# Optimization experiments

Hardware: AMD Instinct MI355X
Metric: run time of the kernel (lower is better)

Reference implementation:

```python
import jax, jax.numpy as jnp
import numpy as np

B, S, DIN, DOUT = 2, 4096, 4096, 11008

def setup_inputs() -> dict:
    key = jax.random.key(0)
    k1, k2, k3 = jax.random.split(key, 3)
    x = jax.random.normal(k1, (B, S, DIN), dtype=jnp.float32)
    # kaiming-uniform-ish full-precision weight
    bound_w = 1.0 / np.sqrt(DIN)
    weight = jax.random.uniform(k2, (DOUT, DIN), dtype=jnp.float32, minval=-bound_w, maxval=bound_w)
    bias = jax.random.uniform(k3, (DOUT,), dtype=jnp.float32, minval=-bound_w, maxval=bound_w)
    return {"x": x, "weight": weight, "bias": bias}

def reference(x, weight, bias):
    # Binarize weight to {-1, 0, +1} via sign (matches torch.sign), scale by mean |w| (detached)
    binary_w = jnp.sign(weight)                                  # [DOUT, DIN]
    scale = jax.lax.stop_gradient(jnp.mean(jnp.abs(weight)))    # scalar
    w_q = binary_w * scale
    # F.linear: x @ w_q.T + bias
    out = jnp.einsum('bsi,oi->bso', x, w_q) + bias               # [B, S, DOUT]
    return out
```

## Files before the change

### kernel.cpp

```cpp
#include <hip/hip_runtime.h>

#define MDIM 8192
#define KDIM 4096
#define NDIM 11008

#define NBLK_W 1024

typedef float f32x4 __attribute__((ext_vector_type(4)));
typedef int   i32x4 __attribute__((ext_vector_type(4)));
typedef char  c4    __attribute__((ext_vector_type(4)));

#define GAS __attribute__((address_space(1)))
#define LAS __attribute__((address_space(3)))

__global__ __launch_bounds__(256) void k_convert_w(const float* __restrict__ w,
                                                   char* __restrict__ wq,
                                                   float* __restrict__ partials) {
  const int n4 = (NDIM * KDIM) / 4;
  const int stride = gridDim.x * blockDim.x;
  float s = 0.f;
  for (int i = blockIdx.x * blockDim.x + threadIdx.x; i < n4; i += stride) {
    f32x4 v = ((const f32x4*)w)[i];
    s += fabsf(v.x) + fabsf(v.y) + fabsf(v.z) + fabsf(v.w);
    c4 q;
    q.x = v.x > 0.f ? 1 : (v.x < 0.f ? -1 : 0);
    q.y = v.y > 0.f ? 1 : (v.y < 0.f ? -1 : 0);
    q.z = v.z > 0.f ? 1 : (v.z < 0.f ? -1 : 0);
    q.w = v.w > 0.f ? 1 : (v.w < 0.f ? -1 : 0);
    ((c4*)wq)[i] = q;
  }
  #pragma unroll
  for (int off = 32; off > 0; off >>= 1) s += __shfl_down(s, off, 64);
  __shared__ float red[4];
  if ((threadIdx.x & 63) == 0) red[threadIdx.x >> 6] = s;
  __syncthreads();
  if (threadIdx.x == 0) partials[blockIdx.x] = red[0] + red[1] + red[2] + red[3];
}

__global__ __launch_bounds__(256) void k_scale(const float* __restrict__ partials,
                                               float* __restrict__ scale) {
  float s = 0.f;
  for (int i = threadIdx.x; i < NBLK_W; i += 256) s += partials[i];
  #pragma unroll
  for (int off = 32; off > 0; off >>= 1) s += __shfl_down(s, off, 64);
  __shared__ float red[4];
  if ((threadIdx.x & 63) == 0) red[threadIdx.x >> 6] = s;
  __syncthreads();
  if (threadIdx.x == 0)
    *scale = (red[0] + red[1] + red[2] + red[3]) / (float)((size_t)NDIM * KDIM);
}

__global__ __launch_bounds__(256) void k_convert_x(const float* __restrict__ x,
                                                   char* __restrict__ xq,
                                                   float* __restrict__ sx) {
  const int row = blockIdx.x;
  const float* xr = x + (size_t)row * KDIM;
  const int t = (int)threadIdx.x;
  f32x4 v[4];
  float mx = 0.f;
  #pragma unroll
  for (int j = 0; j < 4; ++j) {
    v[j] = *(const f32x4*)(xr + j * 1024 + t * 4);
    mx = fmaxf(mx, fmaxf(fmaxf(fabsf(v[j].x), fabsf(v[j].y)),
                         fmaxf(fabsf(v[j].z), fabsf(v[j].w))));
  }
  #pragma unroll
  for (int off = 32; off > 0; off >>= 1) mx = fmaxf(mx, __shfl_xor(mx, off, 64));
  __shared__ float red[4];
  __shared__ float bmax;
  if ((t & 63) == 0) red[t >> 6] = mx;
  __syncthreads();
  if (t == 0) {
    float m2 = fmaxf(fmaxf(red[0], red[1]), fmaxf(red[2], red[3]));
    m2 = fmaxf(m2, 1e-20f);
    bmax = m2;
    sx[row] = m2 * (1.f / 127.f);
  }
  __syncthreads();
  const float r = 127.f / bmax;
  #pragma unroll
  for (int j = 0; j < 4; ++j) {
    int a = __float2int_rn(v[j].x * r), b = __float2int_rn(v[j].y * r);
    int c = __float2int_rn(v[j].z * r), d = __float2int_rn(v[j].w * r);
    a = a > 127 ? 127 : (a < -127 ? -127 : a);
    b = b > 127 ? 127 : (b < -127 ? -127 : b);
    c = c > 127 ? 127 : (c < -127 ? -127 : c);
    d = d > 127 ? 127 : (d < -127 ? -127 : d);
    c4 q; q.x = (char)a; q.y = (char)b; q.z = (char)c; q.w = (char)d;
    *(c4*)(xq + (size_t)row * KDIM + j * 1024 + t * 4) = q;
  }
}


#define BAR()  __builtin_amdgcn_s_barrier()
#define SB0()  __builtin_amdgcn_sched_barrier(0)
#define PRIO1() __builtin_amdgcn_s_setprio(1)
#define PRIO0() __builtin_amdgcn_s_setprio(0)
#define VM(N)  asm volatile("s_waitcnt vmcnt(" #N ")" ::: "memory")

#define STAGE(GP, ROWB, LDSOFF, HALF, KT) do {                                        \
  const char* _s = (GP) + (size_t)((ROWB) + (HALF)*128 + srow) * KDIM                 \
                   + (KT)*64 + scol;                                                  \
  char* _d = lds + (LDSOFF) + (HALF)*8192 + tid*16;                                   \
  __builtin_amdgcn_global_load_lds((const GAS unsigned int*)_s,                       \
                                   (LAS unsigned int*)_d, 16, 0, 0);                  \
} while (0)

#define LOAD_B2(DST, BUF, NB)                                                         \
  _Pragma("unroll") for (int ni = 0; ni < 2; ++ni)                                    \
    DST[ni] = *(const i32x4*)&lds[(BUF)*32768 + 16384 + bWOff + ((NB)+ni)*1024        \
                                  + rowoff + rcol];

#define LOAD_A(DST, BUF, MQ)                                                          \
  _Pragma("unroll") for (int mi = 0; mi < 4; ++mi)                                    \
    DST[mi] = *(const i32x4*)&lds[(BUF)*32768 + aWOff + (MQ)*4096 + mi*1024           \
                                  + rowoff + rcol];

#define MFMA8(AF, MB, BQ, NB)                                                         \
  _Pragma("unroll") for (int mi = 0; mi < 4; ++mi)                                    \
  _Pragma("unroll") for (int ni = 0; ni < 2; ++ni)                                    \
    acc[(MB)+mi][(NB)+ni] = __builtin_amdgcn_mfma_i32_16x16x64_i8(                    \
        AF[mi], BQ[ni], acc[(MB)+mi][(NB)+ni], 0, 0, 0);

__global__ __launch_bounds__(512, 2) void k_gemm256(const char* __restrict__ A,
                                                    const char* __restrict__ B,
                                                    const float* __restrict__ bias,
                                                    const float* __restrict__ sx,
                                                    const float* __restrict__ scale_p,
                                                    float* __restrict__ C) {
  extern __shared__ char lds[];

  const int nTn = NDIM / 256;
  const int nwg = (MDIM / 256) * nTn;
  int wg = (int)blockIdx.x;
  wg = (wg & 7) * (nwg / 8) + (wg >> 3);
  const int tm = wg / nTn;
  const int tn = wg % nTn;

  const int tid  = (int)threadIdx.x;
  const int lane = tid & 63;
  const int wave = tid >> 6;
  const int wm   = wave >> 2;
  const int wn   = wave & 3;
  const int l15  = lane & 15;

  const int rowoff = l15 * 64;
  const int rcol = ((lane >> 4) << 4) ^ (((l15 >> 1) & 3) << 4);
  const int srow = tid >> 2;
  const int scol = ((tid & 3) << 4) ^ (((tid >> 3) & 3) << 4);

  const int aWOff = wm * 8192;
  const int bWOff = (wn >> 1) * 8192 + (wn & 1) * 4096;
  const int aRow = tm * 256;
  const int bRow = tn * 256;

  i32x4 acc[8][4];
  #pragma unroll
  for (int i = 0; i < 8; ++i)
    #pragma unroll
    for (int j = 0; j < 4; ++j) acc[i][j] = i32x4{0, 0, 0, 0};

  i32x4 af[4], bq01[2], bq23[2];

  STAGE(B, bRow, 16384, 0, 0);
  STAGE(B, bRow, 16384, 1, 0);
  STAGE(A, aRow, 0,     0, 0);
  STAGE(A, aRow, 0,     1, 0);
  STAGE(B, bRow, 49152, 0, 1);
  STAGE(B, bRow, 49152, 1, 1);
  VM(2);
  SB0();
  BAR();
  LOAD_A(af, 0, 0); LOAD_B2(bq01, 0, 0);

  #pragma unroll 1
  for (int i = 0; i < 32; ++i) {
    const int kA = 2 * i + 1;
    const int kB = (2 * i + 2 > 63) ? 63 : 2 * i + 2;
    const int kC = (2 * i + 3 > 63) ? 63 : 2 * i + 3;
    PRIO1(); MFMA8(af, 0, bq01, 0); PRIO0(); SB0();
    LOAD_B2(bq23, 0, 2);
    STAGE(A, aRow, 32768, 0, kA);
    BAR();
    PRIO1(); MFMA8(af, 0, bq23, 2); PRIO0(); SB0();
    LOAD_A(af, 0, 1);
    STAGE(A, aRow, 32768, 1, kA);
    BAR();
    PRIO1(); MFMA8(af, 4, bq01, 0); PRIO0(); SB0();
    STAGE(B, bRow, 16384, 0, kB);
    VM(1); SB0();
    BAR();
    PRIO1(); MFMA8(af, 4, bq23, 2); PRIO0(); SB0();
    LOAD_A(af, 1, 0); LOAD_B2(bq01, 1, 0);
    STAGE(B, bRow, 16384, 1, kB);
    BAR();
    PRIO1(); MFMA8(af, 0, bq01, 0); PRIO0(); SB0();
    LOAD_B2(bq23, 1, 2);
    STAGE(A, aRow, 0, 0, kB);
    BAR();
    PRIO1(); MFMA8(af, 0, bq23, 2); PRIO0(); SB0();
    LOAD_A(af, 1, 1);
    STAGE(A, aRow, 0, 1, kB);
    BAR();
    PRIO1(); MFMA8(af, 4, bq01, 0); PRIO0(); SB0();
    STAGE(B, bRow, 49152, 0, kC);
    VM(1); SB0();
    BAR();
    PRIO1(); MFMA8(af, 4, bq23, 2); PRIO0(); SB0();
    LOAD_A(af, 0, 0); LOAD_B2(bq01, 0, 0);
    STAGE(B, bRow, 49152, 1, kC);
    BAR();
  }

  VM(0);

  const float sc = *scale_p;
  float bv[4];
  #pragma unroll
  for (int ni = 0; ni < 4; ++ni) bv[ni] = bias[tn * 256 + wn * 64 + ni * 16 + l15];

  #pragma unroll
  for (int mi = 0; mi < 8; ++mi) {
    #pragma unroll
    for (int r = 0; r < 4; ++r) {
      const int m = tm * 256 + wm * 128 + mi * 16 + (lane >> 4) * 4 + r;
      const float srow_scale = sc * sx[m];
      float* crow = C + (size_t)m * NDIM + tn * 256 + wn * 64;
      #pragma unroll
      for (int ni = 0; ni < 4; ++ni)
        crow[ni * 16 + l15] = srow_scale * (float)acc[mi][ni][r] + bv[ni];
    }
  }
}

extern "C" void kernel_launch(void* const* d_in, const int* in_sizes, int n_in,
                              void* d_out, int out_size, void* d_ws, size_t ws_size,
                              hipStream_t stream) {
  const float* x = (const float*)d_in[0];
  const float* w = (const float*)d_in[1];
  const float* bias = (const float*)d_in[2];
  float* out = (float*)d_out;

  char* ws = (char*)d_ws;
  const size_t XQ_BYTES = (size_t)MDIM * KDIM;
  const size_t WQ_BYTES = (size_t)NDIM * KDIM;
  char* xq = ws;
  char* wq = ws + XQ_BYTES;
  float* sx = (float*)(ws + XQ_BYTES + WQ_BYTES);
  float* partials = sx + MDIM;
  float* scale = partials + NBLK_W;

  k_convert_w<<<NBLK_W, 256, 0, stream>>>(w, wq, partials);
  k_scale<<<1, 256, 0, stream>>>(partials, scale);
  k_convert_x<<<MDIM, 256, 0, stream>>>(x, xq, sx);

  (void)hipFuncSetAttribute((const void*)k_gemm256,
                            hipFuncAttributeMaxDynamicSharedMemorySize, 65536);
  const int grid = (MDIM / 256) * (NDIM / 256);
  k_gemm256<<<grid, 512, 65536, stream>>>(xq, wq, bias, sx, scale, out);
}
```

Before: 506.7 us.

## Shrink GEMM tile to 128x256 and raise occupancy to four workgroups per CU

The int8 GEMM tile shrinks from 256x256 to 128x256, so each wave holds a 64x64 accumulator instead of 128x64 and the LDS footprint drops to 48KB. Launch bounds go up to four workgroups per CU, and the staging schedule is rewritten around the new A/B buffer layout with full vmcnt drains. The goal is more resident waves to hide latency and more tiles to fill the grid. In exchange each tile gets less data reuse, so global and LDS traffic per MFMA roughly doubles, and the VM(0) waits serialise loads more than the earlier VM(1) waits did.

Result: slower. 540.8 us (+6.7%).

```diff
diff --git a/kernel.cpp b/kernel.cpp
--- a/kernel.cpp
+++ b/kernel.cpp
@@ -98,31 +98,30 @@
 #define PRIO0() __builtin_amdgcn_s_setprio(0)
 #define VM(N)  asm volatile("s_waitcnt vmcnt(" #N ")" ::: "memory")
 
-#define STAGE(GP, ROWB, LDSOFF, HALF, KT) do {                                        \
-  const char* _s = (GP) + (size_t)((ROWB) + (HALF)*128 + srow) * KDIM                 \
-                   + (KT)*64 + scol;                                                  \
-  char* _d = lds + (LDSOFF) + (HALF)*8192 + tid*16;                                   \
+#define STAGE(GP, GROWB, LDSBASE, KT) do {                                            \
+  const char* _s = (GP) + (size_t)((GROWB) + srow) * KDIM + (KT)*64 + scol;           \
+  char* _d = lds + (LDSBASE) + tid*16;                                                \
   __builtin_amdgcn_global_load_lds((const GAS unsigned int*)_s,                       \
                                    (LAS unsigned int*)_d, 16, 0, 0);                  \
 } while (0)
 
-#define LOAD_B2(DST, BUF, NB)                                                         \
+#define LOAD_B2(DST, BUF, NH)                                                         \
   _Pragma("unroll") for (int ni = 0; ni < 2; ++ni)                                    \
-    DST[ni] = *(const i32x4*)&lds[(BUF)*32768 + 16384 + bWOff + ((NB)+ni)*1024        \
+    DST[ni] = *(const i32x4*)&lds[(BUF)*24576 + 8192 + bWOff + (NH)*2048 + ni*1024    \
                                   + rowoff + rcol];
 
-#define LOAD_A(DST, BUF, MQ)                                                          \
-  _Pragma("unroll") for (int mi = 0; mi < 4; ++mi)                                    \
-    DST[mi] = *(const i32x4*)&lds[(BUF)*32768 + aWOff + (MQ)*4096 + mi*1024           \
+#define LOAD_A2(DST, BUF, MH)                                                         \
+  _Pragma("unroll") for (int mi = 0; mi < 2; ++mi)                                    \
+    DST[mi] = *(const i32x4*)&lds[(BUF)*24576 + aWOff + (MH)*2048 + mi*1024           \
                                   + rowoff + rcol];
 
-#define MFMA8(AF, MB, BQ, NB)                                                         \
-  _Pragma("unroll") for (int mi = 0; mi < 4; ++mi)                                    \
+#define MFMA4(AF, MB, BQ, NB)                                                         \
+  _Pragma("unroll") for (int mi = 0; mi < 2; ++mi)                                    \
   _Pragma("unroll") for (int ni = 0; ni < 2; ++ni)                                    \
     acc[(MB)+mi][(NB)+ni] = __builtin_amdgcn_mfma_i32_16x16x64_i8(                    \
         AF[mi], BQ[ni], acc[(MB)+mi][(NB)+ni], 0, 0, 0);
 
-__global__ __launch_bounds__(512, 2) void k_gemm256(const char* __restrict__ A,
+__global__ __launch_bounds__(512, 4) void k_gemm256(const char* __restrict__ A,
                                                     const char* __restrict__ B,
                                                     const float* __restrict__ bias,
                                                     const float* __restrict__ sx,
@@ -131,7 +130,7 @@
   extern __shared__ char lds[];
 
   const int nTn = NDIM / 256;
-  const int nwg = (MDIM / 256) * nTn;
+  const int nwg = (MDIM / 128) * nTn;
   int wg = (int)blockIdx.x;
   wg = (wg & 7) * (nwg / 8) + (wg >> 3);
   const int tm = wg / nTn;
@@ -149,66 +148,62 @@
   const int srow = tid >> 2;
   const int scol = ((tid & 3) << 4) ^ (((tid >> 3) & 3) << 4);
 
-  const int aWOff = wm * 8192;
-  const int bWOff = (wn >> 1) * 8192 + (wn & 1) * 4096;
-  const int aRow = tm * 256;
+  const int aWOff = wm * 4096;
+  const int bWOff = wn * 4096;
+  const int aRow = tm * 128;
   const int bRow = tn * 256;
 
-  i32x4 acc[8][4];
-  #pragma unroll
-  for (int i = 0; i < 8; ++i)
+  i32x4 acc[4][4];
+  #pragma unroll
+  for (int i = 0; i < 4; ++i)
     #pragma unroll
     for (int j = 0; j < 4; ++j) acc[i][j] = i32x4{0, 0, 0, 0};
 
-  i32x4 af[4], bq01[2], bq23[2];
-
-  STAGE(B, bRow, 16384, 0, 0);
-  STAGE(B, bRow, 16384, 1, 0);
-  STAGE(A, aRow, 0,     0, 0);
-  STAGE(A, aRow, 0,     1, 0);
-  STAGE(B, bRow, 49152, 0, 1);
-  STAGE(B, bRow, 49152, 1, 1);
-  VM(2);
+  i32x4 af[2], bq01[2], bq23[2];
+
+  STAGE(A, aRow,        0,     0);
+  STAGE(B, bRow,        8192,  0);
+  STAGE(B, bRow + 128,  16384, 0);
+  STAGE(A, aRow,        24576, 1);
+  VM(0);
   SB0();
   BAR();
-  LOAD_A(af, 0, 0); LOAD_B2(bq01, 0, 0);
+  LOAD_A2(af, 0, 0); LOAD_B2(bq01, 0, 0);
 
   #pragma unroll 1
   for (int i = 0; i < 32; ++i) {
     const int kA = 2 * i + 1;
     const int kB = (2 * i + 2 > 63) ? 63 : 2 * i + 2;
     const int kC = (2 * i + 3 > 63) ? 63 : 2 * i + 3;
-    PRIO1(); MFMA8(af, 0, bq01, 0); PRIO0(); SB0();
-    LOAD_B2(bq23, 0, 2);
-    STAGE(A, aRow, 32768, 0, kA);
-    BAR();
-    PRIO1(); MFMA8(af, 0, bq23, 2); PRIO0(); SB0();
-    LOAD_A(af, 0, 1);
-    STAGE(A, aRow, 32768, 1, kA);
-    BAR();
-    PRIO1(); MFMA8(af, 4, bq01, 0); PRIO0(); SB0();
-    STAGE(B, bRow, 16384, 0, kB);
-    VM(1); SB0();
-    BAR();
-    PRIO1(); MFMA8(af, 4, bq23, 2); PRIO0(); SB0();
-    LOAD_A(af, 1, 0); LOAD_B2(bq01, 1, 0);
-    STAGE(B, bRow, 16384, 1, kB);
-    BAR();
-    PRIO1(); MFMA8(af, 0, bq01, 0); PRIO0(); SB0();
-    LOAD_B2(bq23, 1, 2);
-    STAGE(A, aRow, 0, 0, kB);
-    BAR();
-    PRIO1(); MFMA8(af, 0, bq23, 2); PRIO0(); SB0();
-    LOAD_A(af, 1, 1);
-    STAGE(A, aRow, 0, 1, kB);
-    BAR();
-    PRIO1(); MFMA8(af, 4, bq01, 0); PRIO0(); SB0();
-    STAGE(B, bRow, 49152, 0, kC);
-    VM(1); SB0();
-    BAR();
-    PRIO1(); MFMA8(af, 4, bq23, 2); PRIO0(); SB0();
-    LOAD_A(af, 0, 0); LOAD_B2(bq01, 0, 0);
-    STAGE(B, bRow, 49152, 1, kC);
+    PRIO1(); MFMA4(af, 0, bq01, 0); PRIO0(); SB0();
+    LOAD_B2(bq23, 0, 1);
+    STAGE(B, bRow,       32768, kA);
+    BAR();
+    PRIO1(); MFMA4(af, 0, bq23, 2); PRIO0(); SB0();
+    LOAD_A2(af, 0, 1);
+    STAGE(B, bRow + 128, 40960, kA);
+    BAR();
+    PRIO1(); MFMA4(af, 2, bq01, 0); PRIO0(); SB0();
+    VM(0); SB0();
+    BAR();
+    PRIO1(); MFMA4(af, 2, bq23, 2); PRIO0(); SB0();
+    LOAD_A2(af, 1, 0); LOAD_B2(bq01, 1, 0);
+    STAGE(A, aRow,       0,     kB);
+    BAR();
+    PRIO1(); MFMA4(af, 0, bq01, 0); PRIO0(); SB0();
+    LOAD_B2(bq23, 1, 1);
+    STAGE(B, bRow,       8192,  kB);
+    BAR();
+    PRIO1(); MFMA4(af, 0, bq23, 2); PRIO0(); SB0();
+    LOAD_A2(af, 1, 1);
+    STAGE(B, bRow + 128, 16384, kB);
+    BAR();
+    PRIO1(); MFMA4(af, 2, bq01, 0); PRIO0(); SB0();
+    VM(0); SB0();
+    BAR();
+    PRIO1(); MFMA4(af, 2, bq23, 2); PRIO0(); SB0();
+    LOAD_A2(af, 0, 0); LOAD_B2(bq01, 0, 0);
+    STAGE(A, aRow,       24576, kC);
     BAR();
   }
 
@@ -220,10 +215,10 @@
   for (int ni = 0; ni < 4; ++ni) bv[ni] = bias[tn * 256 + wn * 64 + ni * 16 + l15];
 
   #pragma unroll
-  for (int mi = 0; mi < 8; ++mi) {
+  for (int mi = 0; mi < 4; ++mi) {
     #pragma unroll
     for (int r = 0; r < 4; ++r) {
-      const int m = tm * 256 + wm * 128 + mi * 16 + (lane >> 4) * 4 + r;
+      const int m = tm * 128 + wm * 64 + mi * 16 + (lane >> 4) * 4 + r;
       const float srow_scale = sc * sx[m];
       float* crow = C + (size_t)m * NDIM + tn * 256 + wn * 64;
       #pragma unroll
@@ -255,7 +250,7 @@
   k_convert_x<<<MDIM, 256, 0, stream>>>(x, xq, sx);
 
   (void)hipFuncSetAttribute((const void*)k_gemm256,
-                            hipFuncAttributeMaxDynamicSharedMemorySize, 65536);
-  const int grid = (MDIM / 256) * (NDIM / 256);
-  k_gemm256<<<grid, 512, 65536, stream>>>(xq, wq, bias, sx, scale, out);
-}
+                            hipFuncAttributeMaxDynamicSharedMemorySize, 49152);
+  const int grid = (MDIM / 128) * (NDIM / 256);
+  k_gemm256<<<grid, 512, 49152, stream>>>(xq, wq, bias, sx, scale, out);
+}
```
